# Kernel tuning notes

Hardware: AMD Instinct MI355X
Metric: run time of the kernel (lower is better)

## Reference

```python
import jax, jax.numpy as jnp
import numpy as np

TOP_K = 8
N_GROUP = 8
TOPK_GROUP = 4
ROUTED_SCALE = 2.5


def setup_inputs() -> dict:
    key = jax.random.key(0)
    ks = jax.random.split(key, 7)
    T, H, E, I, SI = 4096, 1024, 32, 512, 2048
    W = 0.05  # weight scale to keep relu^2 activations sane
    return {
        "hidden_states": jax.random.normal(ks[0], (T, H), jnp.float32),
        "gate_w": jax.random.normal(ks[1], (E, H), jnp.float32) * W,
        "bias": jax.random.normal(ks[2], (E,), jnp.float32),
        "w_up": jax.random.normal(ks[3], (E, I, H), jnp.float32) * W,
        "w_down": jax.random.normal(ks[4], (E, H, I), jnp.float32) * W,
        "shared_up": jax.random.normal(ks[5], (SI, H), jnp.float32) * W,
        "shared_down": jax.random.normal(ks[6], (H, SI), jnp.float32) * W,
    }


def _grouped_topk_sigmoid(logits, bias):
    # vLLM grouped_topk with scoring_func='sigmoid' + e_score_correction_bias
    T, E = logits.shape
    scores = jax.nn.sigmoid(logits)                       # [T, E]
    sfc = scores + bias[None, :]                          # scores for choice
    g = sfc.reshape(T, N_GROUP, E // N_GROUP)
    group_scores = jnp.sum(jax.lax.top_k(g, 2)[0], -1)    # [T, G] sum of top-2
    grp_idx = jax.lax.top_k(group_scores, TOPK_GROUP)[1]  # [T, topk_group]
    gmask = jnp.zeros((T, N_GROUP), bool).at[jnp.arange(T)[:, None], grp_idx].set(True)
    emask = jnp.repeat(gmask, E // N_GROUP, axis=1)       # [T, E]
    masked = jnp.where(emask, sfc, -jnp.inf)
    topk_ids = jax.lax.top_k(masked, TOP_K)[1]            # [T, K]
    topk_w = jnp.take_along_axis(scores, topk_ids, axis=1)  # weights from raw scores
    topk_w = topk_w / jnp.sum(topk_w, axis=-1, keepdims=True)  # renormalize
    return topk_w, topk_ids


def reference(hidden_states, gate_w, bias, w_up, w_down, shared_up, shared_down):
    x = hidden_states
    T, H = x.shape
    E = gate_w.shape[0]
    # router (fp32 gate)
    logits = x.astype(jnp.float32) @ gate_w.T
    topk_w, topk_ids = _grouped_topk_sigmoid(logits, bias)
    # dense combine weights [T, E] (zero for unselected experts)
    gates = jnp.zeros((T, E), x.dtype).at[jnp.arange(T)[:, None], topk_ids].set(
        topk_w.astype(x.dtype))
    # routed experts: relu^2 MLP (no gating mul), combined with gate weights
    h = jnp.einsum('th,eih->tei', x, w_up)                # [T, E, I]
    h = jnp.square(jax.nn.relu(h))
    routed = jnp.einsum('tei,te,ehi->th', h, gates, w_down)
    # shared expert (same relu^2 MLP)
    s = jnp.square(jax.nn.relu(x @ shared_up.T)) @ shared_down.T
    return routed * ROUTED_SCALE + s
```

## Files before the change

### kernel.cpp

```cpp
#include <hip/hip_runtime.h>
#include <hip/hip_bf16.h>


typedef _Float16 h8 __attribute__((ext_vector_type(8)));
typedef _Float16 h4 __attribute__((ext_vector_type(4)));
typedef float f4 __attribute__((ext_vector_type(4)));

#define T_TOK 4096
#define HDIM  1024
#define NEXP  32
#define IDIM  512
#define SIDIM 2048
#define TOPK  8
#define MAXT256 160

__device__ __forceinline__ void gload16(const void* g, void* l) {
    __builtin_amdgcn_global_load_lds(
        (const __attribute__((address_space(1))) void*)g,
        (__attribute__((address_space(3))) void*)l, 16, 0, 0);
}

__global__ __launch_bounds__(256) void cvt_all_kernel(
    const float* __restrict__ sA, _Float16* __restrict__ dA, int nA,
    const float* __restrict__ sB, _Float16* __restrict__ dB, int nB,
    const float* __restrict__ sC, _Float16* __restrict__ dC, int nC,
    const float* __restrict__ sD, _Float16* __restrict__ dD, int nD,
    const float* __restrict__ sE, _Float16* __restrict__ dE, int nE) {
    const int total = nA + nB + nC + nD + nE;
    for (int gi = blockIdx.x * 256 + threadIdx.x; gi < total; gi += gridDim.x * 256) {
        const float* s; _Float16* d; int i = gi;
        if (i < nA) { s = sA; d = dA; }
        else { i -= nA;
        if (i < nB) { s = sB; d = dB; }
        else { i -= nB;
        if (i < nC) { s = sC; d = dC; }
        else { i -= nC;
        if (i < nD) { s = sD; d = dD; }
        else { i -= nD; s = sE; d = dE; } } } }
        float4 v = reinterpret_cast<const float4*>(s)[i];
        h4 h; h[0] = (_Float16)v.x; h[1] = (_Float16)v.y; h[2] = (_Float16)v.z; h[3] = (_Float16)v.w;
        reinterpret_cast<h4*>(d)[i] = h;
    }
}

__global__ __launch_bounds__(256) void logits_select_kernel(
    const float* __restrict__ x, const float* __restrict__ gw,
    const float* __restrict__ bias, int* __restrict__ topk_ids,
    float* __restrict__ topk_w) {
    const int t0  = blockIdx.x * 16;
    const int tid = threadIdx.x;
    __shared__ double xS[16][66];
    __shared__ double gS[32][65];
    __shared__ double sS[16][33];
    __shared__ double sfcS[16][33];
    const int e  = tid & 31;
    const int tg = tid >> 5;
    const int tA = tg * 2, tB = tg * 2 + 1;
    double acc0 = 0.0, acc1 = 0.0;

    for (int kc = 0; kc < HDIM; kc += 64) {
        {
            int r = tid >> 4, c0 = (tid & 15) * 4;
            float4 v = *reinterpret_cast<const float4*>(x + (size_t)(t0 + r) * HDIM + kc + c0);
            xS[r][c0]     = (double)v.x;
            xS[r][c0 + 1] = (double)v.y;
            xS[r][c0 + 2] = (double)v.z;
            xS[r][c0 + 3] = (double)v.w;
        }
        {
            int r = tid >> 3, c0 = (tid & 7) * 8;
            const float* gp = gw + (size_t)r * HDIM + kc + c0;
            float4 v0 = *reinterpret_cast<const float4*>(gp);
            float4 v1 = *reinterpret_cast<const float4*>(gp + 4);
            gS[r][c0]     = (double)v0.x;
            gS[r][c0 + 1] = (double)v0.y;
            gS[r][c0 + 2] = (double)v0.z;
            gS[r][c0 + 3] = (double)v0.w;
            gS[r][c0 + 4] = (double)v1.x;
            gS[r][c0 + 5] = (double)v1.y;
            gS[r][c0 + 6] = (double)v1.z;
            gS[r][c0 + 7] = (double)v1.w;
        }
        __syncthreads();
#pragma unroll
        for (int k = 0; k < 64; ++k) {
            double g = gS[e][k];
            acc0 = fma(g, xS[tA][k], acc0);
            acc1 = fma(g, xS[tB][k], acc1);
        }
        __syncthreads();
    }
    {
        double s0 = 1.0 / (1.0 + exp(-acc0));
        double s1 = 1.0 / (1.0 + exp(-acc1));
        double b = (double)bias[e];
        sS[tA][e] = s0;  sfcS[tA][e] = s0 + b;
        sS[tB][e] = s1;  sfcS[tB][e] = s1 + b;
    }
    __syncthreads();

    if (tid < 16) {
        const int t = t0 + tid;
        double gsc[8];
        for (int g = 0; g < 8; ++g) {
            double m1 = -1e300, m2 = -1e300;
            for (int j = 0; j < 4; ++j) {
                double v = sfcS[tid][g * 4 + j];
                if (v > m1) { m2 = m1; m1 = v; } else if (v > m2) { m2 = v; }
            }
            gsc[g] = m1 + m2;
        }
        bool gsel[8] = {};
        for (int r = 0; r < 4; ++r) {
            int best = 0; double bv = -1e300;
            for (int g = 0; g < 8; ++g)
                if (!gsel[g] && gsc[g] > bv) { bv = gsc[g]; best = g; }
            gsel[best] = true;
        }
        bool esel[32];
        for (int i2 = 0; i2 < 32; ++i2) esel[i2] = false;
        int ids[8]; double wsum = 0.0;
        for (int r = 0; r < 8; ++r) {
            int best = 0; double bv = -1e300;
            for (int e2 = 0; e2 < 32; ++e2)
                if (gsel[e2 >> 2] && !esel[e2] && sfcS[tid][e2] > bv) { bv = sfcS[tid][e2]; best = e2; }
            esel[best] = true;
            ids[r] = best;
            wsum += sS[tid][best];
        }
        for (int r = 0; r < 8; ++r) {
            topk_ids[t * TOPK + r] = ids[r];
            topk_w[t * TOPK + r] = (float)(sS[tid][ids[r]] / wsum * 2.5);
        }
    }
}

__global__ void build_lists_kernel(const int* __restrict__ ids, const float* __restrict__ w,
                                   int* __restrict__ tok_list, float* __restrict__ wt_list,
                                   int* __restrict__ dest_list, int* __restrict__ counts) {
    const int e = blockIdx.x;
    const int lane = threadIdx.x;
    int base = 0;
    for (int t0 = 0; t0 < T_TOK; t0 += 64) {
        int t = t0 + lane;
        int found = -1;
#pragma unroll
        for (int k = 0; k < TOPK; ++k)
            if (ids[t * TOPK + k] == e) found = k;
        unsigned long long mask = __ballot(found >= 0);
        if (found >= 0) {
            int pos = base + __popcll(mask & ((1ull << lane) - 1ull));
            tok_list[e * T_TOK + pos]  = t;
            wt_list[e * T_TOK + pos]   = w[t * TOPK + found];
            dest_list[e * T_TOK + pos] = t * TOPK + found;
        }
        base += __popcll(mask);
    }
    if (lane == 0) counts[e] = base;
}

__global__ void scan_offsets_kernel(const int* __restrict__ counts, int* __restrict__ offsets,
                                    int* __restrict__ tmap) {
    if (threadIdx.x == 0) {
        int run = 0, nt = 0;
        for (int e = 0; e < NEXP; ++e) {
            offsets[e] = run;
            for (int m0 = 0; m0 < counts[e]; m0 += 256) {
                tmap[1 + 2 * nt] = e;
                tmap[2 + 2 * nt] = m0;
                ++nt;
            }
            run += counts[e];
        }
        offsets[NEXP] = run;
        tmap[0] = nt;
    }
}

template<int K>
__device__ __forceinline__ void gemm256(const _Float16* const (&aP)[4],
                                        const _Float16* const (&bP)[2],
                                        f4 (&acc)[4][4]) {
    __shared__ __attribute__((aligned(16))) _Float16 As[2][256 * 64];
    __shared__ __attribute__((aligned(16))) _Float16 Bs[2][128 * 64];
    const int tid  = threadIdx.x;
    const int w    = tid >> 6, lane = tid & 63;
    const int wm   = (w >> 1) * 64;
    const int wn   = (w & 1) * 64;
    const int ra   = lane & 15, kq = lane >> 4;
    const int nt   = K / 64;

#pragma unroll
    for (int i = 0; i < 4; ++i)
        gload16(aP[i], &As[0][(i * 64 + w * 8) * 64]);
#pragma unroll
    for (int j = 0; j < 2; ++j)
        gload16(bP[j], &Bs[0][(j * 64 + w * 8) * 64]);

    for (int t = 0; t < nt; ++t) {
        const int cur = t & 1;
        if (t + 1 < nt) {
#pragma unroll
            for (int i = 0; i < 4; ++i)
                gload16(aP[i] + (t + 1) * 64, &As[cur ^ 1][(i * 64 + w * 8) * 64]);
#pragma unroll
            for (int j = 0; j < 2; ++j)
                gload16(bP[j] + (t + 1) * 64, &Bs[cur ^ 1][(j * 64 + w * 8) * 64]);
            asm volatile("s_waitcnt vmcnt(6)" ::: "memory");
        } else {
            asm volatile("s_waitcnt vmcnt(0)" ::: "memory");
        }
        __builtin_amdgcn_s_barrier();
        asm volatile("" ::: "memory");

        h8 bF[4][2];
#pragma unroll
        for (int n = 0; n < 4; ++n)
#pragma unroll
            for (int ks = 0; ks < 2; ++ks) {
                int row = wn + n * 16 + ra;
                bF[n][ks] = *reinterpret_cast<const h8*>(
                    &Bs[cur][row * 64 + (((ks * 4 + kq) ^ (ra & 7)) << 3)]);
            }
#pragma unroll
        for (int mh = 0; mh < 2; ++mh) {
            h8 aF[2][2];
#pragma unroll
            for (int mq = 0; mq < 2; ++mq)
#pragma unroll
                for (int ks = 0; ks < 2; ++ks) {
                    int row = wm + mh * 32 + mq * 16 + ra;
                    aF[mq][ks] = *reinterpret_cast<const h8*>(
                        &As[cur][row * 64 + (((ks * 4 + kq) ^ (ra & 7)) << 3)]);
                }
            __builtin_amdgcn_s_setprio(1);
#pragma unroll
            for (int ks = 0; ks < 2; ++ks)
#pragma unroll
                for (int mq = 0; mq < 2; ++mq)
#pragma unroll
                    for (int n = 0; n < 4; ++n)
                        acc[mh * 2 + mq][n] = __builtin_amdgcn_mfma_f32_16x16x32_f16(
                            aF[mq][ks], bF[n][ks], acc[mh * 2 + mq][n], 0, 0, 0);
            __builtin_amdgcn_s_setprio(0);
        }
        asm volatile("" ::: "memory");
        __builtin_amdgcn_s_barrier();
        asm volatile("" ::: "memory");
    }
}

__global__ __launch_bounds__(512, 2) void up_routed_kernel(
    const _Float16* __restrict__ xh, const _Float16* __restrict__ whup,
    const int* __restrict__ tok_list, const float* __restrict__ wt_list,
    const int* __restrict__ counts, const int* __restrict__ offsets,
    const int* __restrict__ tmap, _Float16* __restrict__ hbuf) {
    const int ti = blockIdx.x;
    if (ti >= tmap[0]) return;
    const int e   = tmap[1 + 2 * ti];
    const int m0  = tmap[2 + 2 * ti];
    const int cnt = counts[e];
    const int n0   = blockIdx.y * 128;
    const int eoff = offsets[e];

    __shared__ int   tokS[256];
    __shared__ float wS[256];
    const int tid = threadIdx.x;
    if (tid < 256) {
        int row = m0 + tid;
        int cr  = row < cnt ? row : cnt - 1;
        tokS[tid] = tok_list[e * T_TOK + cr];
        wS[tid]   = row < cnt ? wt_list[e * T_TOK + row] : 0.f;
    }
    __syncthreads();

    const int w = tid >> 6, lane = tid & 63;
    const int swz = ((lane & 7) ^ (lane >> 3)) << 3;
    const int rr  = w * 8 + (lane >> 3);
    const _Float16* aP[4]; const _Float16* bP[2];
#pragma unroll
    for (int i = 0; i < 4; ++i)
        aP[i] = xh + (size_t)tokS[i * 64 + rr] * HDIM + swz;
#pragma unroll
    for (int j = 0; j < 2; ++j)
        bP[j] = whup + ((size_t)e * IDIM + n0 + j * 64 + rr) * HDIM + swz;

    f4 acc[4][4] = {};
    gemm256<HDIM>(aP, bP, acc);

    const int wm = (w >> 1) * 64, wn = (w & 1) * 64;
    const int kq = lane >> 4, cc = lane & 15;
#pragma unroll
    for (int m = 0; m < 4; ++m)
#pragma unroll
    for (int r = 0; r < 4; ++r) {
        int orow = wm + m * 16 + kq * 4 + r;
        if (m0 + orow < cnt) {
            float g = wS[orow];
            size_t rb = (size_t)(eoff + m0 + orow) * IDIM + n0;
#pragma unroll
            for (int n = 0; n < 4; ++n) {
                float v = fmaxf(acc[m][n][r], 0.f);
                hbuf[rb + wn + n * 16 + cc] = (_Float16)(v * v * g);
            }
        }
    }
}

template<bool SLOT>
__global__ __launch_bounds__(512, 2) void down_routed_kernel(
    const _Float16* __restrict__ hbuf, const _Float16* __restrict__ whdown,
    const int* __restrict__ dest_list, const int* __restrict__ counts,
    const int* __restrict__ offsets, const int* __restrict__ tmap,
    _Float16* __restrict__ slotout, float* __restrict__ out) {
    const int ti = blockIdx.x;
    if (ti >= tmap[0]) return;
    const int e   = tmap[1 + 2 * ti];
    const int m0  = tmap[2 + 2 * ti];
    const int cnt = counts[e];
    const int n0   = blockIdx.y * 128;
    const int eoff = offsets[e];

    __shared__ int dS[256];
    const int tid = threadIdx.x;
    if (tid < 256) {
        int row = m0 + tid;
        dS[tid] = dest_list[e * T_TOK + (row < cnt ? row : cnt - 1)];
    }
    __syncthreads();

    const int w = tid >> 6, lane = tid & 63;
    const int swz = ((lane & 7) ^ (lane >> 3)) << 3;
    const int rr  = w * 8 + (lane >> 3);
    const _Float16* aP[4]; const _Float16* bP[2];
#pragma unroll
    for (int i = 0; i < 4; ++i) {
        int row = m0 + i * 64 + rr;
        int cr  = row < cnt ? row : cnt - 1;
        aP[i] = hbuf + (size_t)(eoff + cr) * IDIM + swz;
    }
#pragma unroll
    for (int j = 0; j < 2; ++j)
        bP[j] = whdown + ((size_t)e * HDIM + n0 + j * 64 + rr) * IDIM + swz;

    f4 acc[4][4] = {};
    gemm256<IDIM>(aP, bP, acc);

    const int wm = (w >> 1) * 64, wn = (w & 1) * 64;
    const int kq = lane >> 4, cc = lane & 15;
#pragma unroll
    for (int m = 0; m < 4; ++m)
#pragma unroll
    for (int r = 0; r < 4; ++r) {
        int orow = wm + m * 16 + kq * 4 + r;
        if (m0 + orow < cnt) {
            int d = dS[orow];
            if (SLOT) {
                size_t rb = (size_t)d * HDIM + n0;
#pragma unroll
                for (int n = 0; n < 4; ++n)
                    slotout[rb + wn + n * 16 + cc] = (_Float16)acc[m][n][r];
            } else {
                size_t rb = (size_t)(d >> 3) * HDIM + n0;
#pragma unroll
                for (int n = 0; n < 4; ++n)
                    atomicAdd(&out[rb + wn + n * 16 + cc], acc[m][n][r]);
            }
        }
    }
}

__global__ __launch_bounds__(512, 2) void up_shared_kernel(
    const _Float16* __restrict__ xh, const _Float16* __restrict__ shup,
    _Float16* __restrict__ sh) {
    const int m0 = blockIdx.x * 256;
    const int n0 = blockIdx.y * 128;
    const int tid = threadIdx.x;
    const int w = tid >> 6, lane = tid & 63;
    const int swz = ((lane & 7) ^ (lane >> 3)) << 3;
    const int rr  = w * 8 + (lane >> 3);
    const _Float16* aP[4]; const _Float16* bP[2];
#pragma unroll
    for (int i = 0; i < 4; ++i)
        aP[i] = xh + (size_t)(m0 + i * 64 + rr) * HDIM + swz;
#pragma unroll
    for (int j = 0; j < 2; ++j)
        bP[j] = shup + (size_t)(n0 + j * 64 + rr) * HDIM + swz;

    f4 acc[4][4] = {};
    gemm256<HDIM>(aP, bP, acc);

    const int wm = (w >> 1) * 64, wn = (w & 1) * 64;
    const int kq = lane >> 4, cc = lane & 15;
#pragma unroll
    for (int m = 0; m < 4; ++m)
#pragma unroll
    for (int r = 0; r < 4; ++r) {
        int orow = wm + m * 16 + kq * 4 + r;
        size_t rb = (size_t)(m0 + orow) * SIDIM + n0;
#pragma unroll
        for (int n = 0; n < 4; ++n) {
            float v = fmaxf(acc[m][n][r], 0.f);
            sh[rb + wn + n * 16 + cc] = (_Float16)(v * v);
        }
    }
}

template<int K>
__device__ __forceinline__ void gemm128(const _Float16* const (&aSrc)[4],
                                        const _Float16* const (&bSrc)[4],
                                        f4 (&acc)[4][4]) {
    __shared__ __attribute__((aligned(16))) _Float16 As[128 * 64];
    __shared__ __attribute__((aligned(16))) _Float16 Bs[128 * 64];
    const int tid  = threadIdx.x;
    const int w    = tid >> 6, lane = tid & 63;
    const int wm   = (w & 1) * 64, wn = (w >> 1) * 64;
    const int ra   = lane & 15, kq = lane >> 4;

    for (int kk = 0; kk < K; kk += 64) {
#pragma unroll
        for (int i = 0; i < 4; ++i) {
            gload16(aSrc[i] + kk, As + (size_t)(i * 256 + w * 64) * 8);
            gload16(bSrc[i] + kk, Bs + (size_t)(i * 256 + w * 64) * 8);
        }
        __syncthreads();
#pragma unroll
        for (int s = 0; s < 2; ++s) {
            h8 af[4], bf[4];
#pragma unroll
            for (int m = 0; m < 4; ++m) {
                int row = wm + m * 16 + ra;
                af[m] = *reinterpret_cast<const h8*>(As + row * 64 + (((s * 4 + kq) ^ (row & 7)) << 3));
            }
#pragma unroll
            for (int n = 0; n < 4; ++n) {
                int row = wn + n * 16 + ra;
                bf[n] = *reinterpret_cast<const h8*>(Bs + row * 64 + (((s * 4 + kq) ^ (row & 7)) << 3));
            }
#pragma unroll
            for (int m = 0; m < 4; ++m)
#pragma unroll
                for (int n = 0; n < 4; ++n)
                    acc[m][n] = __builtin_amdgcn_mfma_f32_16x16x32_f16(af[m], bf[n], acc[m][n], 0, 0, 0);
        }
        __syncthreads();
    }
}

template<bool COMB>
__global__ __launch_bounds__(256) void down_shared_kernel(
    const _Float16* __restrict__ sh, const _Float16* __restrict__ shdown,
    const _Float16* __restrict__ slotout, float* __restrict__ out) {
    const int m0 = blockIdx.y * 128;
    const int n0 = blockIdx.x * 128;
    const int tid = threadIdx.x;
    const int sc = ((tid & 7) ^ ((tid >> 3) & 7)) << 3;
    const int r0 = tid >> 3;
    const _Float16* aSrc[4]; const _Float16* bSrc[4];
#pragma unroll
    for (int i = 0; i < 4; ++i) {
        aSrc[i] = sh + (size_t)(m0 + i * 32 + r0) * SIDIM + sc;
        bSrc[i] = shdown + (size_t)(n0 + i * 32 + r0) * SIDIM + sc;
    }
    f4 acc[4][4] = {};
    gemm128<SIDIM>(aSrc, bSrc, acc);

    const int w = tid >> 6, lane = tid & 63;
    const int wm = (w & 1) * 64, wn = (w >> 1) * 64;
    const int cq = lane >> 4, cc = lane & 15;
#pragma unroll
    for (int m = 0; m < 4; ++m)
#pragma unroll
    for (int r = 0; r < 4; ++r) {
        int orow = wm + m * 16 + cq * 4 + r;
        size_t trow = (size_t)(m0 + orow);
#pragma unroll
        for (int n = 0; n < 4; ++n) {
            int col = n0 + wn + n * 16 + cc;
            float v = acc[m][n][r];
            if (COMB) {
                const _Float16* sp = slotout + trow * TOPK * HDIM + col;
#pragma unroll
                for (int k = 0; k < TOPK; ++k)
                    v += (float)sp[(size_t)k * HDIM];
            }
            out[trow * HDIM + col] = v;
        }
    }
}

extern "C" void kernel_launch(void* const* d_in, const int* in_sizes, int n_in,
                              void* d_out, int out_size, void* d_ws, size_t ws_size,
                              hipStream_t stream) {
    const float* x     = (const float*)d_in[0];
    const float* gw    = (const float*)d_in[1];
    const float* bias  = (const float*)d_in[2];
    const float* wup   = (const float*)d_in[3];
    const float* wdown = (const float*)d_in[4];
    const float* sup   = (const float*)d_in[5];
    const float* sdown = (const float*)d_in[6];
    float* out = (float*)d_out;

    char* ws = (char*)d_ws;
    size_t off = 0;
    auto take = [&](size_t bytes) {
        char* p = ws + off;
        off = (off + bytes + 255) & ~(size_t)255;
        return p;
    };
    _Float16* xh      = (_Float16*)take((size_t)T_TOK * HDIM * 2);
    _Float16* whup    = (_Float16*)take((size_t)NEXP * IDIM * HDIM * 2);
    _Float16* whdown  = (_Float16*)take((size_t)NEXP * HDIM * IDIM * 2);
    _Float16* shupW   = (_Float16*)take((size_t)SIDIM * HDIM * 2);
    _Float16* shdownW = (_Float16*)take((size_t)HDIM * SIDIM * 2);
    _Float16* sh      = (_Float16*)take((size_t)T_TOK * SIDIM * 2);
    _Float16* hbuf    = (_Float16*)take((size_t)T_TOK * TOPK * IDIM * 2);
    int*   ids       = (int*)take((size_t)T_TOK * TOPK * 4);
    float* tw        = (float*)take((size_t)T_TOK * TOPK * 4);
    int*   tok_list  = (int*)take((size_t)NEXP * T_TOK * 4);
    float* wt_list   = (float*)take((size_t)NEXP * T_TOK * 4);
    int*   dest_list = (int*)take((size_t)NEXP * T_TOK * 4);
    int*   counts    = (int*)take(NEXP * 4);
    int*   offsets   = (int*)take((NEXP + 1) * 4);
    int*   tmap      = (int*)take((1 + 2 * MAXT256) * 4);
    _Float16* slotout = (_Float16*)take((size_t)T_TOK * TOPK * HDIM * 2);
    const bool use_slot = off <= ws_size;

    logits_select_kernel<<<T_TOK / 16, 256, 0, stream>>>(x, gw, bias, ids, tw);
    build_lists_kernel<<<NEXP, 64, 0, stream>>>(ids, tw, tok_list, wt_list, dest_list, counts);
    scan_offsets_kernel<<<1, 64, 0, stream>>>(counts, offsets, tmap);

    cvt_all_kernel<<<2048, 256, 0, stream>>>(
        x, xh, T_TOK * HDIM / 4,
        wup, whup, NEXP * IDIM * HDIM / 4,
        wdown, whdown, NEXP * HDIM * IDIM / 4,
        sup, shupW, SIDIM * HDIM / 4,
        sdown, shdownW, HDIM * SIDIM / 4);

    up_routed_kernel<<<dim3(MAXT256, IDIM / 128), 512, 0, stream>>>(
        xh, whup, tok_list, wt_list, counts, offsets, tmap, hbuf);
    up_shared_kernel<<<dim3(T_TOK / 256, SIDIM / 128), 512, 0, stream>>>(xh, shupW, sh);

    if (use_slot) {
        down_routed_kernel<true><<<dim3(MAXT256, HDIM / 128), 512, 0, stream>>>(
            hbuf, whdown, dest_list, counts, offsets, tmap, slotout, out);
        down_shared_kernel<true><<<dim3(HDIM / 128, T_TOK / 128), 256, 0, stream>>>(
            sh, shdownW, slotout, out);
    } else {
        down_shared_kernel<false><<<dim3(HDIM / 128, T_TOK / 128), 256, 0, stream>>>(
            sh, shdownW, slotout, out);
        down_routed_kernel<false><<<dim3(MAXT256, HDIM / 128), 512, 0, stream>>>(
            hbuf, whdown, dest_list, counts, offsets, tmap, slotout, out);
    }
}
```

Measured before the change: 347.5 us.

## Use 256x256 GEMM tiles with interleaved prefetch and merge shared-up into routed-up launch

```diff
diff --git a/kernel.cpp b/kernel.cpp
--- a/kernel.cpp
+++ b/kernel.cpp
@@ -12,7 +12,8 @@
 #define IDIM  512
 #define SIDIM 2048
 #define TOPK  8
-#define MAXT256 160
+#define MAXTU 224
+#define MAXTD 160
 
 __device__ __forceinline__ void gload16(const void* g, void* l) {
     __builtin_amdgcn_global_load_lds(
@@ -160,88 +161,136 @@
 }
 
 __global__ void scan_offsets_kernel(const int* __restrict__ counts, int* __restrict__ offsets,
-                                    int* __restrict__ tmap) {
+                                    int* __restrict__ tmapU, int* __restrict__ tmapD) {
     if (threadIdx.x == 0) {
-        int run = 0, nt = 0;
+        int run = 0, ntu = 0, ntd = 0;
         for (int e = 0; e < NEXP; ++e) {
             offsets[e] = run;
             for (int m0 = 0; m0 < counts[e]; m0 += 256) {
-                tmap[1 + 2 * nt] = e;
-                tmap[2 + 2 * nt] = m0;
-                ++nt;
+                tmapU[1 + 2 * ntu] = e; tmapU[2 + 2 * ntu] = m0; ++ntu;
+                tmapD[1 + 2 * ntd] = e; tmapD[2 + 2 * ntd] = m0; ++ntd;
             }
             run += counts[e];
         }
         offsets[NEXP] = run;
-        tmap[0] = nt;
-    }
-}
-
-template<int K>
-__device__ __forceinline__ void gemm256(const _Float16* const (&aP)[4],
-                                        const _Float16* const (&bP)[2],
-                                        f4 (&acc)[4][4]) {
+        for (int c = 0; c < 4; ++c)
+            for (int m0 = 0; m0 < T_TOK; m0 += 256) {
+                tmapU[1 + 2 * ntu] = NEXP + c; tmapU[2 + 2 * ntu] = m0; ++ntu;
+            }
+        tmapU[0] = ntu;
+        tmapD[0] = ntd;
+    }
+}
+
+__device__ __forceinline__ void gemm8p(const _Float16* const (&aP)[4],
+                                       const _Float16* const (&bP)[4],
+                                       const int nt, f4 (&acc)[8][4]) {
     __shared__ __attribute__((aligned(16))) _Float16 As[2][256 * 64];
-    __shared__ __attribute__((aligned(16))) _Float16 Bs[2][128 * 64];
-    const int tid  = threadIdx.x;
-    const int w    = tid >> 6, lane = tid & 63;
-    const int wm   = (w >> 1) * 64;
-    const int wn   = (w & 1) * 64;
-    const int ra   = lane & 15, kq = lane >> 4;
-    const int nt   = K / 64;
-
-#pragma unroll
-    for (int i = 0; i < 4; ++i)
-        gload16(aP[i], &As[0][(i * 64 + w * 8) * 64]);
-#pragma unroll
-    for (int j = 0; j < 2; ++j)
-        gload16(bP[j], &Bs[0][(j * 64 + w * 8) * 64]);
+    __shared__ __attribute__((aligned(16))) _Float16 Bs[2][256 * 64];
+    const int tid = threadIdx.x;
+    const int w = tid >> 6, lane = tid & 63;
+    const int wr = w >> 2, wc = w & 3;
+    const int ra = lane & 15, kq = lane >> 4;
+    const int ldsb = w * 512;
+    const int arow = wr * 128 + ra;
+    const int brow = wc * 64 + ra;
+    const int ch0 = (kq ^ (ra & 7)) << 3;
+    const int ch1 = ((4 + kq) ^ (ra & 7)) << 3;
+
+#pragma unroll
+    for (int j = 0; j < 4; ++j) gload16(aP[j], &As[0][j * 4096 + ldsb]);
+#pragma unroll
+    for (int j = 0; j < 4; ++j) gload16(bP[j], &Bs[0][j * 4096 + ldsb]);
 
     for (int t = 0; t < nt; ++t) {
-        const int cur = t & 1;
-        if (t + 1 < nt) {
-#pragma unroll
-            for (int i = 0; i < 4; ++i)
-                gload16(aP[i] + (t + 1) * 64, &As[cur ^ 1][(i * 64 + w * 8) * 64]);
-#pragma unroll
-            for (int j = 0; j < 2; ++j)
-                gload16(bP[j] + (t + 1) * 64, &Bs[cur ^ 1][(j * 64 + w * 8) * 64]);
-            asm volatile("s_waitcnt vmcnt(6)" ::: "memory");
+        const int buf = t & 1, nb = buf ^ 1;
+        const bool pf = (t + 1 < nt);
+        const int ko = (t + 1) * 64;
+        h8 bf[4];
+
+        if (pf) {
+            gload16(aP[0] + ko, &As[nb][0 * 4096 + ldsb]);
+            gload16(aP[1] + ko, &As[nb][1 * 4096 + ldsb]);
+            asm volatile("s_waitcnt vmcnt(2)" ::: "memory");
         } else {
             asm volatile("s_waitcnt vmcnt(0)" ::: "memory");
         }
         __builtin_amdgcn_s_barrier();
         asm volatile("" ::: "memory");
-
-        h8 bF[4][2];
-#pragma unroll
-        for (int n = 0; n < 4; ++n)
-#pragma unroll
-            for (int ks = 0; ks < 2; ++ks) {
-                int row = wn + n * 16 + ra;
-                bF[n][ks] = *reinterpret_cast<const h8*>(
-                    &Bs[cur][row * 64 + (((ks * 4 + kq) ^ (ra & 7)) << 3)]);
-            }
-#pragma unroll
-        for (int mh = 0; mh < 2; ++mh) {
-            h8 aF[2][2];
-#pragma unroll
-            for (int mq = 0; mq < 2; ++mq)
-#pragma unroll
-                for (int ks = 0; ks < 2; ++ks) {
-                    int row = wm + mh * 32 + mq * 16 + ra;
-                    aF[mq][ks] = *reinterpret_cast<const h8*>(
-                        &As[cur][row * 64 + (((ks * 4 + kq) ^ (ra & 7)) << 3)]);
-                }
+        {
+#pragma unroll
+            for (int n = 0; n < 4; ++n)
+                bf[n] = *reinterpret_cast<const h8*>(&Bs[buf][(brow + n * 16) * 64 + ch0]);
+            h8 af[4];
+#pragma unroll
+            for (int m = 0; m < 4; ++m)
+                af[m] = *reinterpret_cast<const h8*>(&As[buf][(arow + m * 16) * 64 + ch0]);
             __builtin_amdgcn_s_setprio(1);
 #pragma unroll
-            for (int ks = 0; ks < 2; ++ks)
-#pragma unroll
-                for (int mq = 0; mq < 2; ++mq)
-#pragma unroll
-                    for (int n = 0; n < 4; ++n)
-                        acc[mh * 2 + mq][n] = __builtin_amdgcn_mfma_f32_16x16x32_f16(
-                            aF[mq][ks], bF[n][ks], acc[mh * 2 + mq][n], 0, 0, 0);
+            for (int m = 0; m < 4; ++m)
+#pragma unroll
+                for (int n = 0; n < 4; ++n)
+                    acc[m][n] = __builtin_amdgcn_mfma_f32_16x16x32_f16(af[m], bf[n], acc[m][n], 0, 0, 0);
+            __builtin_amdgcn_s_setprio(0);
+        }
+        __builtin_amdgcn_sched_barrier(0);
+
+        if (pf) {
+            gload16(aP[2] + ko, &As[nb][2 * 4096 + ldsb]);
+            gload16(aP[3] + ko, &As[nb][3 * 4096 + ldsb]);
+        }
+        {
+            h8 af[4];
+#pragma unroll
+            for (int m = 0; m < 4; ++m)
+                af[m] = *reinterpret_cast<const h8*>(&As[buf][(arow + (m + 4) * 16) * 64 + ch0]);
+            __builtin_amdgcn_s_setprio(1);
+#pragma unroll
+            for (int m = 0; m < 4; ++m)
+#pragma unroll
+                for (int n = 0; n < 4; ++n)
+                    acc[m + 4][n] = __builtin_amdgcn_mfma_f32_16x16x32_f16(af[m], bf[n], acc[m + 4][n], 0, 0, 0);
+            __builtin_amdgcn_s_setprio(0);
+        }
+        __builtin_amdgcn_sched_barrier(0);
+
+        if (pf) {
+            gload16(bP[0] + ko, &Bs[nb][0 * 4096 + ldsb]);
+            gload16(bP[1] + ko, &Bs[nb][1 * 4096 + ldsb]);
+        }
+        {
+#pragma unroll
+            for (int n = 0; n < 4; ++n)
+                bf[n] = *reinterpret_cast<const h8*>(&Bs[buf][(brow + n * 16) * 64 + ch1]);
+            h8 af[4];
+#pragma unroll
+            for (int m = 0; m < 4; ++m)
+                af[m] = *reinterpret_cast<const h8*>(&As[buf][(arow + m * 16) * 64 + ch1]);
+            __builtin_amdgcn_s_setprio(1);
+#pragma unroll
+            for (int m = 0; m < 4; ++m)
+#pragma unroll
+                for (int n = 0; n < 4; ++n)
+                    acc[m][n] = __builtin_amdgcn_mfma_f32_16x16x32_f16(af[m], bf[n], acc[m][n], 0, 0, 0);
+            __builtin_amdgcn_s_setprio(0);
+        }
+        __builtin_amdgcn_sched_barrier(0);
+
+        if (pf) {
+            gload16(bP[2] + ko, &Bs[nb][2 * 4096 + ldsb]);
+            gload16(bP[3] + ko, &Bs[nb][3 * 4096 + ldsb]);
+        }
+        {
+            h8 af[4];
+#pragma unroll
+            for (int m = 0; m < 4; ++m)
+                af[m] = *reinterpret_cast<const h8*>(&As[buf][(arow + (m + 4) * 16) * 64 + ch1]);
+            __builtin_amdgcn_s_setprio(1);
+#pragma unroll
+            for (int m = 0; m < 4; ++m)
+#pragma unroll
+                for (int n = 0; n < 4; ++n)
+                    acc[m + 4][n] = __builtin_amdgcn_mfma_f32_16x16x32_f16(af[m], bf[n], acc[m + 4][n], 0, 0, 0);
             __builtin_amdgcn_s_setprio(0);
         }
         asm volatile("" ::: "memory");
@@ -250,58 +299,67 @@
     }
 }
 
-__global__ __launch_bounds__(512, 2) void up_routed_kernel(
+__global__ __launch_bounds__(512, 2) void up_kernel(
     const _Float16* __restrict__ xh, const _Float16* __restrict__ whup,
+    const _Float16* __restrict__ shupW,
     const int* __restrict__ tok_list, const float* __restrict__ wt_list,
     const int* __restrict__ counts, const int* __restrict__ offsets,
-    const int* __restrict__ tmap, _Float16* __restrict__ hbuf) {
+    const int* __restrict__ tmap,
+    _Float16* __restrict__ hbuf, _Float16* __restrict__ shb) {
     const int ti = blockIdx.x;
     if (ti >= tmap[0]) return;
-    const int e   = tmap[1 + 2 * ti];
-    const int m0  = tmap[2 + 2 * ti];
-    const int cnt = counts[e];
-    const int n0   = blockIdx.y * 128;
-    const int eoff = offsets[e];
+    const int e  = tmap[1 + 2 * ti];
+    const int m0 = tmap[2 + 2 * ti];
+    const int n0 = blockIdx.y * 256;
+    const bool routed = e < NEXP;
+    const int cnt = routed ? counts[e] : T_TOK;
 
     __shared__ int   tokS[256];
     __shared__ float wS[256];
     const int tid = threadIdx.x;
     if (tid < 256) {
         int row = m0 + tid;
-        int cr  = row < cnt ? row : cnt - 1;
-        tokS[tid] = tok_list[e * T_TOK + cr];
-        wS[tid]   = row < cnt ? wt_list[e * T_TOK + row] : 0.f;
+        int cr = row < cnt ? row : cnt - 1;
+        if (routed) {
+            tokS[tid] = tok_list[e * T_TOK + cr];
+            wS[tid]   = row < cnt ? wt_list[e * T_TOK + row] : 0.f;
+        } else {
+            tokS[tid] = cr;
+            wS[tid]   = 1.f;
+        }
     }
     __syncthreads();
 
     const int w = tid >> 6, lane = tid & 63;
     const int swz = ((lane & 7) ^ (lane >> 3)) << 3;
-    const int rr  = w * 8 + (lane >> 3);
-    const _Float16* aP[4]; const _Float16* bP[2];
-#pragma unroll
-    for (int i = 0; i < 4; ++i)
-        aP[i] = xh + (size_t)tokS[i * 64 + rr] * HDIM + swz;
-#pragma unroll
-    for (int j = 0; j < 2; ++j)
-        bP[j] = whup + ((size_t)e * IDIM + n0 + j * 64 + rr) * HDIM + swz;
-
-    f4 acc[4][4] = {};
-    gemm256<HDIM>(aP, bP, acc);
-
-    const int wm = (w >> 1) * 64, wn = (w & 1) * 64;
-    const int kq = lane >> 4, cc = lane & 15;
-#pragma unroll
-    for (int m = 0; m < 4; ++m)
+    const int rr = w * 8 + (lane >> 3);
+    const _Float16* bbase = routed ? (whup + (size_t)e * IDIM * HDIM)
+                                   : (shupW + (size_t)(e - NEXP) * 512 * HDIM);
+    const _Float16* aP[4]; const _Float16* bP[4];
+#pragma unroll
+    for (int j = 0; j < 4; ++j) {
+        aP[j] = xh + (size_t)tokS[j * 64 + rr] * HDIM + swz;
+        bP[j] = bbase + (size_t)(n0 + j * 64 + rr) * HDIM + swz;
+    }
+    f4 acc[8][4] = {};
+    gemm8p(aP, bP, HDIM / 64, acc);
+
+    const int wr = w >> 2, wc = w & 3;
+    const int kq = lane >> 4, ra = lane & 15;
+    _Float16* obase; size_t ostr;
+    if (routed) { obase = hbuf + (size_t)(offsets[e] + m0) * IDIM + n0; ostr = IDIM; }
+    else        { obase = shb + (size_t)m0 * SIDIM + (size_t)(e - NEXP) * 512 + n0; ostr = SIDIM; }
+#pragma unroll
+    for (int m = 0; m < 8; ++m)
 #pragma unroll
     for (int r = 0; r < 4; ++r) {
-        int orow = wm + m * 16 + kq * 4 + r;
+        int orow = wr * 128 + m * 16 + kq * 4 + r;
         if (m0 + orow < cnt) {
             float g = wS[orow];
-            size_t rb = (size_t)(eoff + m0 + orow) * IDIM + n0;
 #pragma unroll
             for (int n = 0; n < 4; ++n) {
                 float v = fmaxf(acc[m][n][r], 0.f);
-                hbuf[rb + wn + n * 16 + cc] = (_Float16)(v * v * g);
+                obase[(size_t)orow * ostr + wc * 64 + n * 16 + ra] = (_Float16)(v * v * g);
             }
         }
     }
@@ -318,7 +376,7 @@
     const int e   = tmap[1 + 2 * ti];
     const int m0  = tmap[2 + 2 * ti];
     const int cnt = counts[e];
-    const int n0   = blockIdx.y * 128;
+    const int n0   = blockIdx.y * 256;
     const int eoff = offsets[e];
 
     __shared__ int dS[256];
@@ -331,77 +389,38 @@
 
     const int w = tid >> 6, lane = tid & 63;
     const int swz = ((lane & 7) ^ (lane >> 3)) << 3;
-    const int rr  = w * 8 + (lane >> 3);
-    const _Float16* aP[4]; const _Float16* bP[2];
-#pragma unroll
-    for (int i = 0; i < 4; ++i) {
-        int row = m0 + i * 64 + rr;
+    const int rr = w * 8 + (lane >> 3);
+    const _Float16* aP[4]; const _Float16* bP[4];
+#pragma unroll
+    for (int j = 0; j < 4; ++j) {
+        int row = m0 + j * 64 + rr;
         int cr  = row < cnt ? row : cnt - 1;
-        aP[i] = hbuf + (size_t)(eoff + cr) * IDIM + swz;
-    }
-#pragma unroll
-    for (int j = 0; j < 2; ++j)
+        aP[j] = hbuf + (size_t)(eoff + cr) * IDIM + swz;
         bP[j] = whdown + ((size_t)e * HDIM + n0 + j * 64 + rr) * IDIM + swz;
-
-    f4 acc[4][4] = {};
-    gemm256<IDIM>(aP, bP, acc);
-
-    const int wm = (w >> 1) * 64, wn = (w & 1) * 64;
-    const int kq = lane >> 4, cc = lane & 15;
-#pragma unroll
-    for (int m = 0; m < 4; ++m)
+    }
+    f4 acc[8][4] = {};
+    gemm8p(aP, bP, IDIM / 64, acc);
+
+    const int wr = w >> 2, wc = w & 3;
+    const int kq = lane >> 4, ra = lane & 15;
+#pragma unroll
+    for (int m = 0; m < 8; ++m)
 #pragma unroll
     for (int r = 0; r < 4; ++r) {
-        int orow = wm + m * 16 + kq * 4 + r;
+        int orow = wr * 128 + m * 16 + kq * 4 + r;
         if (m0 + orow < cnt) {
             int d = dS[orow];
             if (SLOT) {
                 size_t rb = (size_t)d * HDIM + n0;
 #pragma unroll
                 for (int n = 0; n < 4; ++n)
-                    slotout[rb + wn + n * 16 + cc] = (_Float16)acc[m][n][r];
+                    slotout[rb + wc * 64 + n * 16 + ra] = (_Float16)acc[m][n][r];
             } else {
                 size_t rb = (size_t)(d >> 3) * HDIM + n0;
 #pragma unroll
                 for (int n = 0; n < 4; ++n)
-                    atomicAdd(&out[rb + wn + n * 16 + cc], acc[m][n][r]);
-            }
-        }
-    }
-}
-
-__global__ __launch_bounds__(512, 2) void up_shared_kernel(
-    const _Float16* __restrict__ xh, const _Float16* __restrict__ shup,
-    _Float16* __restrict__ sh) {
-    const int m0 = blockIdx.x * 256;
-    const int n0 = blockIdx.y * 128;
-    const int tid = threadIdx.x;
-    const int w = tid >> 6, lane = tid & 63;
-    const int swz = ((lane & 7) ^ (lane >> 3)) << 3;
-    const int rr  = w * 8 + (lane >> 3);
-    const _Float16* aP[4]; const _Float16* bP[2];
-#pragma unroll
-    for (int i = 0; i < 4; ++i)
-        aP[i] = xh + (size_t)(m0 + i * 64 + rr) * HDIM + swz;
-#pragma unroll
-    for (int j = 0; j < 2; ++j)
-        bP[j] = shup + (size_t)(n0 + j * 64 + rr) * HDIM + swz;
-
-    f4 acc[4][4] = {};
-    gemm256<HDIM>(aP, bP, acc);
-
-    const int wm = (w >> 1) * 64, wn = (w & 1) * 64;
-    const int kq = lane >> 4, cc = lane & 15;
-#pragma unroll
-    for (int m = 0; m < 4; ++m)
-#pragma unroll
-    for (int r = 0; r < 4; ++r) {
-        int orow = wm + m * 16 + kq * 4 + r;
-        size_t rb = (size_t)(m0 + orow) * SIDIM + n0;
-#pragma unroll
-        for (int n = 0; n < 4; ++n) {
-            float v = fmaxf(acc[m][n][r], 0.f);
-            sh[rb + wn + n * 16 + cc] = (_Float16)(v * v);
+                    atomicAdd(&out[rb + wc * 64 + n * 16 + ra], acc[m][n][r]);
+            }
         }
     }
 }
@@ -522,13 +541,14 @@
     int*   dest_list = (int*)take((size_t)NEXP * T_TOK * 4);
     int*   counts    = (int*)take(NEXP * 4);
     int*   offsets   = (int*)take((NEXP + 1) * 4);
-    int*   tmap      = (int*)take((1 + 2 * MAXT256) * 4);
+    int*   tmapU     = (int*)take((1 + 2 * MAXTU) * 4);
+    int*   tmapD     = (int*)take((1 + 2 * MAXTD) * 4);
     _Float16* slotout = (_Float16*)take((size_t)T_TOK * TOPK * HDIM * 2);
     const bool use_slot = off <= ws_size;
 
     logits_select_kernel<<<T_TOK / 16, 256, 0, stream>>>(x, gw, bias, ids, tw);
     build_lists_kernel<<<NEXP, 64, 0, stream>>>(ids, tw, tok_list, wt_list, dest_list, counts);
-    scan_offsets_kernel<<<1, 64, 0, stream>>>(counts, offsets, tmap);
+    scan_offsets_kernel<<<1, 64, 0, stream>>>(counts, offsets, tmapU, tmapD);
 
     cvt_all_kernel<<<2048, 256, 0, stream>>>(
         x, xh, T_TOK * HDIM / 4,
@@ -537,19 +557,18 @@
         sup, shupW, SIDIM * HDIM / 4,
         sdown, shdownW, HDIM * SIDIM / 4);
 
-    up_routed_kernel<<<dim3(MAXT256, IDIM / 128), 512, 0, stream>>>(
-        xh, whup, tok_list, wt_list, counts, offsets, tmap, hbuf);
-    up_shared_kernel<<<dim3(T_TOK / 256, SIDIM / 128), 512, 0, stream>>>(xh, shupW, sh);
+    up_kernel<<<dim3(MAXTU, 2), 512, 0, stream>>>(
+        xh, whup, shupW, tok_list, wt_list, counts, offsets, tmapU, hbuf, sh);
 
     if (use_slot) {
-        down_routed_kernel<true><<<dim3(MAXT256, HDIM / 128), 512, 0, stream>>>(
-            hbuf, whdown, dest_list, counts, offsets, tmap, slotout, out);
+        down_routed_kernel<true><<<dim3(MAXTD, HDIM / 256), 512, 0, stream>>>(
+            hbuf, whdown, dest_list, counts, offsets, tmapD, slotout, out);
         down_shared_kernel<true><<<dim3(HDIM / 128, T_TOK / 128), 256, 0, stream>>>(
             sh, shdownW, slotout, out);
     } else {
         down_shared_kernel<false><<<dim3(HDIM / 128, T_TOK / 128), 256, 0, stream>>>(
             sh, shdownW, slotout, out);
-        down_routed_kernel<false><<<dim3(MAXT256, HDIM / 128), 512, 0, stream>>>(
-            hbuf, whdown, dest_list, counts, offsets, tmap, slotout, out);
-    }
-}
+        down_routed_kernel<false><<<dim3(MAXTD, HDIM / 256), 512, 0, stream>>>(
+            hbuf, whdown, dest_list, counts, offsets, tmapD, slotout, out);
+    }
+}
```

New measurement: 325.8 us. 1.07x faster.
